# Performance work log

Hardware: AMD Instinct MI355X
Metric: run time of the kernel (lower is better)

## Reference

```python
import jax, jax.numpy as jnp
import numpy as np

HID = 128


def setup_inputs() -> dict:
    key = jax.random.key(0)
    ks = jax.random.split(key, 7)
    B = 131072
    X = jax.random.normal(ks[0], (B, 4), dtype=jnp.float32)
    # Linear params stored as (in, out); scaled ~ 1/sqrt(fan_in) like torch default
    W1 = jax.random.normal(ks[1], (4, HID), dtype=jnp.float32) * 0.5
    b1 = jnp.zeros((HID,), jnp.float32)
    W2 = jax.random.normal(ks[2], (HID, HID), dtype=jnp.float32) * (1.0 / np.sqrt(HID))
    b2 = jnp.zeros((HID,), jnp.float32)
    W3 = jax.random.normal(ks[3], (HID, 1), dtype=jnp.float32) * (1.0 / np.sqrt(HID))
    b3 = jnp.zeros((1,), jnp.float32)
    return {"X": X, "W1": W1, "b1": b1, "W2": W2, "b2": b2, "W3": W3, "b3": b3}


def reference(X, W1, b1, W2, b2, W3, b3):
    def V_fn(feat):  # feat: [4] -> scalar potential
        h = jnp.tanh(feat @ W1 + b1)
        h = jnp.tanh(h @ W2 + b2)
        return (h @ W3 + b3)[0]

    def L_single(q, qd):  # q:[2], qd:[2] -> scalar Lagrangian
        t1, t2 = q[0], q[1]
        w1, w2 = qd[0], qd[1]
        T = w1 ** 2 + 0.5 * w2 ** 2 + w1 * w2 * jnp.cos(t1 - t2)
        feat = jnp.stack([jnp.sin(t1), jnp.cos(t1), jnp.sin(t2), jnp.cos(t2)])
        return T - V_fn(feat)

    q = X[:, :2]
    qd = X[:, 2:]
    dL_dq = jax.vmap(jax.grad(L_single, argnums=0))(q, qd)          # [B,2]
    # mass matrix M[i,j] = d^2 L / (d qd_i d qd_j)
    M = jax.vmap(jax.jacfwd(jax.grad(L_single, argnums=1), argnums=1))(q, qd)  # [B,2,2]
    # cross Hessian H[i,j] = d^2 L / (d qd_i d q_j); Coriolis C_i = H[i,:] @ qd
    H = jax.vmap(jax.jacfwd(jax.grad(L_single, argnums=1), argnums=0))(q, qd)  # [B,2,2]
    C = jnp.einsum('bij,bj->bi', H, qd)                              # [B,2]
    qdd = jnp.linalg.solve(M, (dL_dq - C)[..., None])[..., 0]        # [B,2]
    return jnp.concatenate([qd, qdd], axis=1)                        # [B,4]
```

## Files before the change

### kernel.cpp

```cpp
#include <hip/hip_runtime.h>
#include <math.h>

#define HID 128
#define TPB 512
#define NW  8
#define GRIDB 512

typedef __bf16 bf16;
typedef bf16 bf16x8 __attribute__((ext_vector_type(8)));
typedef bf16 bf16x4 __attribute__((ext_vector_type(4)));
typedef float floatx4 __attribute__((ext_vector_type(4)));

__device__ __forceinline__ floatx4 tanh4(floatx4 z) {
    floatx4 t = z * 2.885390081777927f;
    floatx4 e = { __builtin_amdgcn_exp2f(t[0]), __builtin_amdgcn_exp2f(t[1]),
                  __builtin_amdgcn_exp2f(t[2]), __builtin_amdgcn_exp2f(t[3]) };
    e = e + 1.0f;
    floatx4 r = { __builtin_amdgcn_rcpf(e[0]), __builtin_amdgcn_rcpf(e[1]),
                  __builtin_amdgcn_rcpf(e[2]), __builtin_amdgcn_rcpf(e[3]) };
    return 1.0f - 2.0f * r;
}


__global__ __launch_bounds__(TPB, 4)
void lnn_kernel(const float* __restrict__ X,
                const float* __restrict__ W1,
                const float* __restrict__ b1,
                const float* __restrict__ b2,
                const float* __restrict__ W3,
                const float* __restrict__ W2,
                float* __restrict__ out,
                int B, int nchunk)
{
    __shared__ __align__(16) bf16 sW2A[16384];
    __shared__ __align__(16) bf16 sW2R[16384];
    __shared__ __align__(16) bf16 sXf[NW][512];
    __shared__ __align__(16) bf16 sW1A[4][512];
    __shared__ __align__(16) float sW1r[4][HID];
    __shared__ __align__(16) float sB1[HID], sB2[HID], sW3[HID];

    const int tid  = threadIdx.x;
    const int w    = tid >> 6;
    const int lane = tid & 63;
    const int lrow = lane & 15;
    const int lq   = lane >> 4;
    const int swz  = lrow & 3;

    { int r = tid >> 7, j = tid & (HID - 1); sW1r[r][j] = W1[r * HID + j]; }
    if (tid < HID) sB1[tid] = b1[tid];
    else if (tid < 2 * HID) sB2[tid - HID] = b2[tid - HID];
    else if (tid < 3 * HID) sW3[tid - 2 * HID] = W3[tid - 2 * HID];

    #pragma unroll
    for (int tt = 0; tt < 4; ++tt) {
        int e = tid + tt * TPB;
        int t = e >> 6, l = e & 63;
        int a = t >> 2, bidx = t & 3;
        int lr = l & 15, q = l >> 4;
        bf16x8 f;
        #pragma unroll
        for (int idx = 0; idx < 8; ++idx)
            f[idx] = (bf16)W2[(32*bidx + 8*q + idx) * HID + 16*a + lr];
        *reinterpret_cast<bf16x8*>(&sW2A[e * 8]) = f;
        const float4* rp = reinterpret_cast<const float4*>(&W2[(16*a + lr) * HID + 32*bidx + 8*q]);
        float4 r0 = rp[0], r1 = rp[1];
        bf16x8 g;
        g[0]=(bf16)r0.x; g[1]=(bf16)r0.y; g[2]=(bf16)r0.z; g[3]=(bf16)r0.w;
        g[4]=(bf16)r1.x; g[5]=(bf16)r1.y; g[6]=(bf16)r1.z; g[7]=(bf16)r1.w;
        *reinterpret_cast<bf16x8*>(&sW2R[e * 8]) = g;
    }
    if (tid < 256) {
        int m = tid >> 6, l = tid & 63;
        int lr = l & 15, q = l >> 4;
        bf16x8 f = {};
        if (lr < 4) {
            #pragma unroll
            for (int idx = 0; idx < 8; ++idx)
                f[idx] = (bf16)W1[lr * HID + 32*m + 8*q + idx];
        }
        *reinterpret_cast<bf16x8*>(&sW1A[m][l * 8]) = f;
    }
    __syncthreads();

    bf16* const lb = &sXf[w][0];
    const int tileStride = GRIDB * NW;
    const int t0 = (int)blockIdx.x * NW + w;
    const floatx4 fz = floatx4{0.f,0.f,0.f,0.f};

    #pragma unroll 1
    for (int c = 0; c < nchunk; ++c) {
        const int tile = t0 + c * tileStride;
        if (tile * 16 >= B) break;
        const int S0 = tile * 16;

        int gc = S0 + lrow; gc = gc < B ? gc : (B - 1);
        float4 xc = reinterpret_cast<const float4*>(X)[gc];
        float s1c, c1c, s2c, c2c;
        __sincosf(xc.x, &s1c, &c1c);
        __sincosf(xc.y, &s2c, &c2c);

        bf16x8 bregc[4];
        #pragma unroll
        for (int kt = 0; kt < 4; ++kt) {
            int jb = 32 * kt + 8 * lq;
            floatx4 w0a = *reinterpret_cast<const floatx4*>(&sW1r[0][jb]);
            floatx4 w0b = *reinterpret_cast<const floatx4*>(&sW1r[0][jb+4]);
            floatx4 w1a = *reinterpret_cast<const floatx4*>(&sW1r[1][jb]);
            floatx4 w1b = *reinterpret_cast<const floatx4*>(&sW1r[1][jb+4]);
            floatx4 w2a = *reinterpret_cast<const floatx4*>(&sW1r[2][jb]);
            floatx4 w2b = *reinterpret_cast<const floatx4*>(&sW1r[2][jb+4]);
            floatx4 w3a = *reinterpret_cast<const floatx4*>(&sW1r[3][jb]);
            floatx4 w3b = *reinterpret_cast<const floatx4*>(&sW1r[3][jb+4]);
            floatx4 bba = *reinterpret_cast<const floatx4*>(&sB1[jb]);
            floatx4 bbb = *reinterpret_cast<const floatx4*>(&sB1[jb+4]);
            floatx4 za = bba + s1c*w0a + c1c*w1a + s2c*w2a + c2c*w3a;
            floatx4 zb = bbb + s1c*w0b + c1c*w1b + s2c*w2b + c2c*w3b;
            floatx4 ha = tanh4(za), hb = tanh4(zb);
            bf16x8 hf;
            hf[0]=(bf16)ha[0]; hf[1]=(bf16)ha[1]; hf[2]=(bf16)ha[2]; hf[3]=(bf16)ha[3];
            hf[4]=(bf16)hb[0]; hf[5]=(bf16)hb[1]; hf[6]=(bf16)hb[2]; hf[7]=(bf16)hb[3];
            bregc[kt] = hf;
        }

        bf16x8 gB[4];
        #pragma unroll
        for (int L = 0; L < 4; ++L) {
            #pragma unroll
            for (int b = 0; b < 2; ++b) {
                int jt = 2*L + b;
                __builtin_amdgcn_s_setprio(1);
                floatx4 acc = __builtin_amdgcn_mfma_f32_16x16x32_bf16(
                    *reinterpret_cast<const bf16x8*>(&sW2A[((jt*4 + 0)*64 + lane)*8]),
                    bregc[0], fz, 0,0,0);
                #pragma unroll
                for (int kt = 1; kt < 4; ++kt)
                    acc = __builtin_amdgcn_mfma_f32_16x16x32_bf16(
                        *reinterpret_cast<const bf16x8*>(&sW2A[((jt*4 + kt)*64 + lane)*8]),
                        bregc[kt], acc, 0,0,0);
                __builtin_amdgcn_s_setprio(0);
                int jb = 16*jt + 4*lq;
                floatx4 b2v = *reinterpret_cast<const floatx4*>(&sB2[jb]);
                floatx4 w3v = *reinterpret_cast<const floatx4*>(&sW3[jb]);
                floatx4 h = tanh4(acc + b2v);
                floatx4 gv = (1.0f - h*h) * w3v;
                bf16x4 g;
                g[0]=(bf16)gv[0]; g[1]=(bf16)gv[1]; g[2]=(bf16)gv[2]; g[3]=(bf16)gv[3];
                int blk = (2*b + (lq>>1)) ^ swz;
                *reinterpret_cast<bf16x4*>(&lb[lrow*32 + blk*8 + 4*(lq&1)]) = g;
            }
            gB[L] = *reinterpret_cast<const bf16x8*>(&lb[lrow*32 + (lq ^ swz)*8]);
        }

        floatx4 dv = fz;
        #pragma unroll
        for (int L = 0; L < 4; ++L) {
            #pragma unroll
            for (int b = 0; b < 2; ++b) {
                int it = 2*L + b;
                __builtin_amdgcn_s_setprio(1);
                floatx4 acc2 = __builtin_amdgcn_mfma_f32_16x16x32_bf16(
                    *reinterpret_cast<const bf16x8*>(&sW2R[((it*4 + 0)*64 + lane)*8]),
                    gB[0], fz, 0,0,0);
                #pragma unroll
                for (int jt2 = 1; jt2 < 4; ++jt2)
                    acc2 = __builtin_amdgcn_mfma_f32_16x16x32_bf16(
                        *reinterpret_cast<const bf16x8*>(&sW2R[((it*4 + jt2)*64 + lane)*8]),
                        gB[jt2], acc2, 0,0,0);
                __builtin_amdgcn_s_setprio(0);
                bf16x4 g;
                g[0]=(bf16)acc2[0]; g[1]=(bf16)acc2[1];
                g[2]=(bf16)acc2[2]; g[3]=(bf16)acc2[3];
                int blk = (2*b + (lq>>1)) ^ swz;
                *reinterpret_cast<bf16x4*>(&lb[lrow*32 + blk*8 + 4*(lq&1)]) = g;
            }
            bf16x8 sv = *reinterpret_cast<const bf16x8*>(&lb[lrow*32 + (lq ^ swz)*8]);
            bf16x8 A3 = *reinterpret_cast<const bf16x8*>(&sW1A[L][lane*8]);
            bf16x8 g1;
            #pragma unroll
            for (int idx = 0; idx < 8; ++idx) {
                float h = (float)bregc[L][idx];
                float s = (float)sv[idx];
                g1[idx] = (bf16)(s - s*h*h);
            }
            __builtin_amdgcn_s_setprio(1);
            dv = __builtin_amdgcn_mfma_f32_16x16x32_bf16(A3, g1, dv, 0,0,0);
            __builtin_amdgcn_s_setprio(0);
        }

        if (lane < 16 && S0 + lane < B) {
            float dV0 = dv[0], dV1 = dv[1], dV2 = dv[2], dV3 = dv[3];
            float cosD = c1c * c2c + s1c * s2c;
            float sinD = s1c * c2c - c1c * s2c;
            float dVt1 = dV0 * c1c - dV1 * s1c;
            float dVt2 = dV2 * c2c - dV3 * s2c;
            float qd1 = xc.z, qd2 = xc.w;
            float sT = qd1 * qd2 * sinD;
            float cw = sinD * (qd2 - qd1);
            float rhs1 = (-sT - dVt1) - qd2 * cw;
            float rhs2 = ( sT - dVt2) - qd1 * cw;
            float det = 2.0f - cosD * cosD;
            float inv = __builtin_amdgcn_rcpf(det);
            float qdd1 = (rhs1 - cosD * rhs2) * inv;
            float qdd2 = (2.0f * rhs2 - cosD * rhs1) * inv;
            *reinterpret_cast<float4*>(&out[4 * (S0 + lane)]) = make_float4(qd1, qd2, qdd1, qdd2);
        }
    }
}

extern "C" void kernel_launch(void* const* d_in, const int* in_sizes, int n_in,
                              void* d_out, int out_size, void* d_ws, size_t ws_size,
                              hipStream_t stream) {
    const float* X  = (const float*)d_in[0];
    const float* W1 = (const float*)d_in[1];
    const float* b1 = (const float*)d_in[2];
    const float* W2 = (const float*)d_in[3];
    const float* b2 = (const float*)d_in[4];
    const float* W3 = (const float*)d_in[5];
    float* out = (float*)d_out;
    int B = in_sizes[0] / 4;
    int tiles = (B + 15) >> 4;
    int nchunk = (tiles + GRIDB * NW - 1) / (GRIDB * NW);
    lnn_kernel<<<GRIDB, TPB, 0, stream>>>(X, W1, b1, b2, W3, W2, out, B, nchunk);
}
```

Baseline: 86.84 us.

## Pre-pack W2 fragments in a prep kernel and read them from global memory

Adds a small prep kernel that converts W2 to bf16 MFMA fragment layouts once into workspace. The main kernel drops its two 32KB shared W2 buffers and per-block conversion, reading fragments from global/L2 instead. The grid is doubled to 1024 blocks, since the smaller LDS footprint allows more resident blocks. The trade-off is that every MFMA operand now comes through the vector memory/cache path instead of LDS, plus one extra kernel launch.

```diff
diff --git a/kernel.cpp b/kernel.cpp
--- a/kernel.cpp
+++ b/kernel.cpp
@@ -4,7 +4,7 @@
 #define HID 128
 #define TPB 512
 #define NW  8
-#define GRIDB 512
+#define GRIDB 1024
 
 typedef __bf16 bf16;
 typedef bf16 bf16x8 __attribute__((ext_vector_type(8)));
@@ -22,18 +22,43 @@
 }
 
 
+__global__ __launch_bounds__(256)
+void prep_kernel(const float* __restrict__ W2, bf16* __restrict__ ws)
+{
+    int e = (int)blockIdx.x * 256 + threadIdx.x;
+    if (e < 2048) {
+        int t = e >> 6, l = e & 63;
+        int jt = t >> 2, kt = t & 3;
+        int lr = l & 15, q = l >> 4;
+        bf16x8 f;
+        #pragma unroll
+        for (int idx = 0; idx < 8; ++idx)
+            f[idx] = (bf16)W2[(32*kt + 8*q + idx) * HID + 16*jt + lr];
+        *reinterpret_cast<bf16x8*>(&ws[e * 8]) = f;
+    } else {
+        int e2 = e - 2048;
+        int t = e2 >> 6, l = e2 & 63;
+        int it = t >> 2, jt2 = t & 3;
+        int lr = l & 15, q = l >> 4;
+        const float4* rp = reinterpret_cast<const float4*>(&W2[(16*it + lr) * HID + 32*jt2 + 8*q]);
+        float4 r0 = rp[0], r1 = rp[1];
+        bf16x8 g;
+        g[0]=(bf16)r0.x; g[1]=(bf16)r0.y; g[2]=(bf16)r0.z; g[3]=(bf16)r0.w;
+        g[4]=(bf16)r1.x; g[5]=(bf16)r1.y; g[6]=(bf16)r1.z; g[7]=(bf16)r1.w;
+        *reinterpret_cast<bf16x8*>(&ws[16384 + e2 * 8]) = g;
+    }
+}
+
 __global__ __launch_bounds__(TPB, 4)
 void lnn_kernel(const float* __restrict__ X,
                 const float* __restrict__ W1,
                 const float* __restrict__ b1,
                 const float* __restrict__ b2,
                 const float* __restrict__ W3,
-                const float* __restrict__ W2,
+                const bf16* __restrict__ ws,
                 float* __restrict__ out,
                 int B, int nchunk)
 {
-    __shared__ __align__(16) bf16 sW2A[16384];
-    __shared__ __align__(16) bf16 sW2R[16384];
     __shared__ __align__(16) bf16 sXf[NW][512];
     __shared__ __align__(16) bf16 sW1A[4][512];
     __shared__ __align__(16) float sW1r[4][HID];
@@ -46,29 +71,13 @@
     const int lq   = lane >> 4;
     const int swz  = lrow & 3;
 
+    const bf16* const wsA = ws;
+    const bf16* const wsR = ws + 16384;
+
     { int r = tid >> 7, j = tid & (HID - 1); sW1r[r][j] = W1[r * HID + j]; }
     if (tid < HID) sB1[tid] = b1[tid];
     else if (tid < 2 * HID) sB2[tid - HID] = b2[tid - HID];
     else if (tid < 3 * HID) sW3[tid - 2 * HID] = W3[tid - 2 * HID];
-
-    #pragma unroll
-    for (int tt = 0; tt < 4; ++tt) {
-        int e = tid + tt * TPB;
-        int t = e >> 6, l = e & 63;
-        int a = t >> 2, bidx = t & 3;
-        int lr = l & 15, q = l >> 4;
-        bf16x8 f;
-        #pragma unroll
-        for (int idx = 0; idx < 8; ++idx)
-            f[idx] = (bf16)W2[(32*bidx + 8*q + idx) * HID + 16*a + lr];
-        *reinterpret_cast<bf16x8*>(&sW2A[e * 8]) = f;
-        const float4* rp = reinterpret_cast<const float4*>(&W2[(16*a + lr) * HID + 32*bidx + 8*q]);
-        float4 r0 = rp[0], r1 = rp[1];
-        bf16x8 g;
-        g[0]=(bf16)r0.x; g[1]=(bf16)r0.y; g[2]=(bf16)r0.z; g[3]=(bf16)r0.w;
-        g[4]=(bf16)r1.x; g[5]=(bf16)r1.y; g[6]=(bf16)r1.z; g[7]=(bf16)r1.w;
-        *reinterpret_cast<bf16x8*>(&sW2R[e * 8]) = g;
-    }
     if (tid < 256) {
         int m = tid >> 6, l = tid & 63;
         int lr = l & 15, q = l >> 4;
@@ -130,12 +139,12 @@
                 int jt = 2*L + b;
                 __builtin_amdgcn_s_setprio(1);
                 floatx4 acc = __builtin_amdgcn_mfma_f32_16x16x32_bf16(
-                    *reinterpret_cast<const bf16x8*>(&sW2A[((jt*4 + 0)*64 + lane)*8]),
+                    *reinterpret_cast<const bf16x8*>(&wsA[((jt*4 + 0)*64 + lane)*8]),
                     bregc[0], fz, 0,0,0);
                 #pragma unroll
                 for (int kt = 1; kt < 4; ++kt)
                     acc = __builtin_amdgcn_mfma_f32_16x16x32_bf16(
-                        *reinterpret_cast<const bf16x8*>(&sW2A[((jt*4 + kt)*64 + lane)*8]),
+                        *reinterpret_cast<const bf16x8*>(&wsA[((jt*4 + kt)*64 + lane)*8]),
                         bregc[kt], acc, 0,0,0);
                 __builtin_amdgcn_s_setprio(0);
                 int jb = 16*jt + 4*lq;
@@ -159,12 +168,12 @@
                 int it = 2*L + b;
                 __builtin_amdgcn_s_setprio(1);
                 floatx4 acc2 = __builtin_amdgcn_mfma_f32_16x16x32_bf16(
-                    *reinterpret_cast<const bf16x8*>(&sW2R[((it*4 + 0)*64 + lane)*8]),
+                    *reinterpret_cast<const bf16x8*>(&wsR[((it*4 + 0)*64 + lane)*8]),
                     gB[0], fz, 0,0,0);
                 #pragma unroll
                 for (int jt2 = 1; jt2 < 4; ++jt2)
                     acc2 = __builtin_amdgcn_mfma_f32_16x16x32_bf16(
-                        *reinterpret_cast<const bf16x8*>(&sW2R[((it*4 + jt2)*64 + lane)*8]),
+                        *reinterpret_cast<const bf16x8*>(&wsR[((it*4 + jt2)*64 + lane)*8]),
                         gB[jt2], acc2, 0,0,0);
                 __builtin_amdgcn_s_setprio(0);
                 bf16x4 g;
@@ -217,8 +226,10 @@
     const float* b2 = (const float*)d_in[4];
     const float* W3 = (const float*)d_in[5];
     float* out = (float*)d_out;
+    bf16* ws = (bf16*)d_ws;
     int B = in_sizes[0] / 4;
     int tiles = (B + 15) >> 4;
     int nchunk = (tiles + GRIDB * NW - 1) / (GRIDB * NW);
-    lnn_kernel<<<GRIDB, TPB, 0, stream>>>(X, W1, b1, b2, W3, W2, out, B, nchunk);
-}
+    prep_kernel<<<16, 256, 0, stream>>>(W2, ws);
+    lnn_kernel<<<GRIDB, TPB, 0, stream>>>(X, W1, b1, b2, W3, ws, out, B, nchunk);
+}
```

Measured after the change: 146.5 us. 1.69x slower.
